# Kernel optimization log

Measured on AMD Instinct MI355X. Metric: run time of the kernel, lower is better.

Reference implementation:

```python
import jax, jax.numpy as jnp
import numpy as np

ALPHA = 1.702
LIMIT = 7.0
TOP_K = 4
NUM_EXPERTS = 16


def setup_inputs() -> dict:
    key = jax.random.key(0)
    ks = jax.random.split(key, 7)
    B, S, H, D, E = 2, 2048, 2048, 2048, NUM_EXPERTS
    return {
        "hidden_states": jax.random.normal(ks[0], (B, S, H), jnp.float32),
        "router_weight": jax.random.normal(ks[1], (E, H), jnp.float32) * 0.02,
        "router_bias": jax.random.normal(ks[2], (E,), jnp.float32) * 0.02,
        "gate_up_proj": jax.random.normal(ks[3], (E, H, 2 * D), jnp.float32) * 0.02,
        "gate_up_proj_bias": jax.random.normal(ks[4], (E, 2 * D), jnp.float32) * 0.02,
        "down_proj": jax.random.normal(ks[5], (E, D, H), jnp.float32) * 0.02,
        "down_proj_bias": jax.random.normal(ks[6], (E, H), jnp.float32) * 0.02,
    }


def _moe(x, gate_up_proj, gate_up_proj_bias, down_proj, down_proj_bias, w_te):
    # x: [T,H]; w_te: [T,E] combine weights (zero for unrouted token/expert pairs)
    T, H = x.shape

    def step(acc, params):
        Wgu, bgu, Wd, bd, we = params  # we: [T]
        gate_up = x @ Wgu + bgu                       # [T, 2D]
        gate, up = jnp.split(gate_up, 2, axis=-1)
        gate = jnp.minimum(gate, LIMIT)               # clamp(max=limit)
        up = jnp.clip(up, -LIMIT, LIMIT)
        glu = gate * jax.nn.sigmoid(gate * ALPHA)
        gated = (up + 1.0) * glu                      # [T, D]
        out = gated @ Wd + bd                         # [T, H]
        return acc + out * we[:, None], None

    acc, _ = jax.lax.scan(
        step,
        jnp.zeros((T, H), jnp.float32),
        (gate_up_proj, gate_up_proj_bias, down_proj, down_proj_bias, w_te.T),
    )
    return acc


def reference(hidden_states, router_weight, router_bias, gate_up_proj,
              gate_up_proj_bias, down_proj, down_proj_bias):
    B, S, H = hidden_states.shape
    x = hidden_states.reshape(-1, H).astype(jnp.float32)  # [T,H]
    T = x.shape[0]

    # Router
    logits = x @ router_weight.T + router_bias            # [T,E]
    top_vals, top_idx = jax.lax.top_k(logits, TOP_K)      # [T,K]
    scores = jax.nn.softmax(top_vals, axis=-1) / TOP_K    # [T,K]

    # Scatter per-token top-k scores into dense [T,E] combine weights
    w_te = jnp.zeros((T, NUM_EXPERTS), jnp.float32)
    w_te = w_te.at[jnp.arange(T)[:, None], top_idx].add(scores)

    y = _moe(x, gate_up_proj, gate_up_proj_bias, down_proj, down_proj_bias, w_te)
    y = y * TOP_K                                         # MLP multiplies by num_experts_per_tok
    y = y.reshape(B, S, H).astype(hidden_states.dtype)
    return y, scores
```

## Files before the change

### kernel.cpp

```cpp
#include <hip/hip_runtime.h>
#include <hip/hip_bf16.h>
#include <math.h>

#define T_TOK 4096
#define H_DIM 2048
#define D_DIM 2048
#define TWO_D 4096
#define E_NUM 16
#define NPAIR (T_TOK * 4)

typedef __attribute__((ext_vector_type(8))) short v8s;
typedef __attribute__((ext_vector_type(4))) float v4f;

__device__ __forceinline__ ushort f2bf(float f) {
    union { float f; unsigned u; } v; v.f = f;
    unsigned u = v.u + 0x7fffu + ((v.u >> 16) & 1u);
    return (ushort)(u >> 16);
}
__device__ __forceinline__ float bf2f(ushort b) {
    union { unsigned u; float f; } v; v.u = ((unsigned)b) << 16;
    return v.f;
}

__global__ void k_convert_x(const float* __restrict__ x, ushort* __restrict__ xb) {
    size_t i = ((size_t)blockIdx.x * 256 + threadIdx.x) * 4;
    float4 v = *(const float4*)(x + i);
    ushort4 o = make_ushort4(f2bf(v.x), f2bf(v.y), f2bf(v.z), f2bf(v.w));
    *(ushort4*)(xb + i) = o;
}

__global__ void k_router(const float* __restrict__ x, const float* __restrict__ rw,
                         const float* __restrict__ rb, float* __restrict__ logits) {
    int t = blockIdx.x;
    int e = threadIdx.x >> 4;
    int j = threadIdx.x & 15;
    const float* xr = x + (size_t)t * H_DIM;
    const float* wr = rw + (size_t)e * H_DIM;
    float s = 0.f;
    #pragma unroll 8
    for (int h = j; h < H_DIM; h += 16) s += xr[h] * wr[h];
    #pragma unroll
    for (int d = 8; d >= 1; d >>= 1) s += __shfl_down(s, d, 16);
    if (j == 0) logits[t * E_NUM + e] = s + rb[e];
}

__global__ void k_topk(const float* __restrict__ logits, float* __restrict__ scores_out,
                       int* __restrict__ tk_e, float* __restrict__ tk_w,
                       int* __restrict__ counts) {
    int t = blockIdx.x * 256 + threadIdx.x;
    if (t >= T_TOK) return;
    float lg[E_NUM];
    #pragma unroll
    for (int e = 0; e < E_NUM; e++) lg[e] = logits[t * E_NUM + e];
    int sel[4]; float sv[4];
    unsigned used = 0;
    #pragma unroll
    for (int k = 0; k < 4; k++) {
        float best = -INFINITY; int bi = 0;
        #pragma unroll
        for (int e = 0; e < E_NUM; e++) {
            if (!((used >> e) & 1) && lg[e] > best) { best = lg[e]; bi = e; }
        }
        used |= 1u << bi; sel[k] = bi; sv[k] = best;
    }
    float m = sv[0];
    float ex[4]; float sum = 0.f;
    #pragma unroll
    for (int k = 0; k < 4; k++) { ex[k] = __expf(sv[k] - m); sum += ex[k]; }
    float inv = 1.f / sum;
    #pragma unroll
    for (int k = 0; k < 4; k++) {
        float w = ex[k] * inv;
        scores_out[t * 4 + k] = w * 0.25f;
        tk_e[t * 4 + k] = sel[k];
        tk_w[t * 4 + k] = w;
        atomicAdd(&counts[sel[k]], 1);
    }
}

__global__ void k_scan(const int* __restrict__ counts, int* __restrict__ offsets) {
    if (threadIdx.x == 0) {
        int s = 0;
        for (int e = 0; e < E_NUM; e++) { offsets[e] = s; s += counts[e]; }
        offsets[E_NUM] = s;
    }
}

__global__ void k_scatter(const int* __restrict__ tk_e, const int* __restrict__ offsets,
                          int* __restrict__ fill, int* __restrict__ pair_token,
                          int* __restrict__ slot_of) {
    int i = blockIdx.x * 256 + threadIdx.x;
    if (i >= NPAIR) return;
    int e = tk_e[i];
    int pos = offsets[e] + atomicAdd(&fill[e], 1);
    pair_token[pos] = i >> 2;
    slot_of[i] = pos;
}

#define BM 128
#define BN 128
#define BK 64
#define LDT 72

__global__ __launch_bounds__(256) void k_gemm1(
    const ushort* __restrict__ xb, const float* __restrict__ Wgu,
    const float* __restrict__ bgu, const int* __restrict__ offsets,
    const int* __restrict__ pair_token, ushort* __restrict__ gu)
{
    __shared__ ushort As[BM * LDT];
    __shared__ ushort Bs[BN * LDT];
    __shared__ int rowtok[BM];

    const int e = blockIdx.z;
    const int off = offsets[e];
    const int cnt = offsets[e + 1] - off;
    const int m0 = blockIdx.y * BM;
    if (m0 >= cnt) return;
    const int n0 = blockIdx.x * BN;
    const int tid = threadIdx.x;

    if (tid < BM) {
        int r = m0 + tid; if (r >= cnt) r = cnt - 1;
        rowtok[tid] = pair_token[off + r];
    }

    const float* W = Wgu + (size_t)e * H_DIM * TWO_D + n0;

    v4f acc[4][4];
    #pragma unroll
    for (int i = 0; i < 4; i++)
        #pragma unroll
        for (int j = 0; j < 4; j++) acc[i][j] = (v4f){0.f, 0.f, 0.f, 0.f};

    const int lane = tid & 63;
    const int wm = ((tid >> 6) & 1) * 64;
    const int wn = (tid >> 7) * 64;
    const int lm = lane & 15;
    const int kg = lane >> 4;

    for (int kb = 0; kb < H_DIM; kb += BK) {
        __syncthreads();
        #pragma unroll
        for (int i = 0; i < 4; i++) {
            int c = tid + 256 * i;
            int row = c >> 3, cq = c & 7;
            const ushort* src = xb + (size_t)rowtok[row] * H_DIM + kb + cq * 8;
            *(uint4*)&As[row * LDT + cq * 8] = *(const uint4*)src;
        }
        #pragma unroll
        for (int i = 0; i < 2; i++) {
            int blk = tid + 256 * i;
            int kb4 = blk >> 5, nb4 = blk & 31;
            const float* wp = W + (size_t)(kb + kb4 * 4) * TWO_D + nb4 * 4;
            float4 r0 = *(const float4*)wp;
            float4 r1 = *(const float4*)(wp + TWO_D);
            float4 r2 = *(const float4*)(wp + 2 * TWO_D);
            float4 r3 = *(const float4*)(wp + 3 * TWO_D);
            ushort* bp = &Bs[(nb4 * 4) * LDT + kb4 * 4];
            *(ushort4*)bp             = make_ushort4(f2bf(r0.x), f2bf(r1.x), f2bf(r2.x), f2bf(r3.x));
            *(ushort4*)(bp + LDT)     = make_ushort4(f2bf(r0.y), f2bf(r1.y), f2bf(r2.y), f2bf(r3.y));
            *(ushort4*)(bp + 2 * LDT) = make_ushort4(f2bf(r0.z), f2bf(r1.z), f2bf(r2.z), f2bf(r3.z));
            *(ushort4*)(bp + 3 * LDT) = make_ushort4(f2bf(r0.w), f2bf(r1.w), f2bf(r2.w), f2bf(r3.w));
        }
        __syncthreads();
        #pragma unroll
        for (int ks = 0; ks < 2; ks++) {
            v8s af[4], bfr[4];
            #pragma unroll
            for (int mi = 0; mi < 4; mi++)
                af[mi] = *(const v8s*)&As[(wm + mi * 16 + lm) * LDT + ks * 32 + kg * 8];
            #pragma unroll
            for (int ni = 0; ni < 4; ni++)
                bfr[ni] = *(const v8s*)&Bs[(wn + ni * 16 + lm) * LDT + ks * 32 + kg * 8];
            #pragma unroll
            for (int mi = 0; mi < 4; mi++)
                #pragma unroll
                for (int ni = 0; ni < 4; ni++)
                    acc[mi][ni] = __builtin_amdgcn_mfma_f32_16x16x32_bf16(af[mi], bfr[ni], acc[mi][ni], 0, 0, 0);
        }
    }

    const float* bias = bgu + (size_t)e * TWO_D + n0;
    #pragma unroll
    for (int mi = 0; mi < 4; mi++) {
        int rbase = wm + mi * 16 + kg * 4;
        #pragma unroll
        for (int ni = 0; ni < 4; ni++) {
            int nl = wn + ni * 16 + lm;
            float bv = bias[nl];
            #pragma unroll
            for (int v = 0; v < 4; v++) {
                int r = rbase + v;
                if (m0 + r < cnt)
                    gu[(size_t)(off + m0 + r) * TWO_D + n0 + nl] = f2bf(acc[mi][ni][v] + bv);
            }
        }
    }
}

__global__ void k_act(const ushort* __restrict__ gu, ushort* __restrict__ gated) {
    int i = blockIdx.x * 256 + threadIdx.x;
    int pr = i >> 9;
    int q = (i & 511) * 4;
    const ushort* grow = gu + (size_t)pr * TWO_D;
    ushort4 g4 = *(const ushort4*)(grow + q);
    ushort4 u4 = *(const ushort4*)(grow + D_DIM + q);
    float g[4] = { bf2f(g4.x), bf2f(g4.y), bf2f(g4.z), bf2f(g4.w) };
    float u[4] = { bf2f(u4.x), bf2f(u4.y), bf2f(u4.z), bf2f(u4.w) };
    ushort o[4];
    #pragma unroll
    for (int j = 0; j < 4; j++) {
        float gate = fminf(g[j], 7.f);
        float up = fminf(fmaxf(u[j], -7.f), 7.f);
        float glu = gate / (1.f + __expf(-1.702f * gate));
        o[j] = f2bf((up + 1.f) * glu);
    }
    *(ushort4*)(gated + (size_t)pr * D_DIM + q) = make_ushort4(o[0], o[1], o[2], o[3]);
}

__global__ __launch_bounds__(256) void k_gemm2(
    const ushort* __restrict__ gated, const float* __restrict__ Wd,
    const float* __restrict__ bd, const int* __restrict__ offsets,
    ushort* __restrict__ po)
{
    __shared__ ushort As[BM * LDT];
    __shared__ ushort Bs[BN * LDT];

    const int e = blockIdx.z;
    const int off = offsets[e];
    const int cnt = offsets[e + 1] - off;
    const int m0 = blockIdx.y * BM;
    if (m0 >= cnt) return;
    const int n0 = blockIdx.x * BN;
    const int tid = threadIdx.x;

    const float* W = Wd + (size_t)e * D_DIM * H_DIM + n0;

    v4f acc[4][4];
    #pragma unroll
    for (int i = 0; i < 4; i++)
        #pragma unroll
        for (int j = 0; j < 4; j++) acc[i][j] = (v4f){0.f, 0.f, 0.f, 0.f};

    const int lane = tid & 63;
    const int wm = ((tid >> 6) & 1) * 64;
    const int wn = (tid >> 7) * 64;
    const int lm = lane & 15;
    const int kg = lane >> 4;

    for (int kb = 0; kb < D_DIM; kb += BK) {
        __syncthreads();
        #pragma unroll
        for (int i = 0; i < 4; i++) {
            int c = tid + 256 * i;
            int row = c >> 3, cq = c & 7;
            int gr = m0 + row; if (gr >= cnt) gr = cnt - 1;
            const ushort* src = gated + (size_t)(off + gr) * D_DIM + kb + cq * 8;
            *(uint4*)&As[row * LDT + cq * 8] = *(const uint4*)src;
        }
        #pragma unroll
        for (int i = 0; i < 2; i++) {
            int blk = tid + 256 * i;
            int kb4 = blk >> 5, nb4 = blk & 31;
            const float* wp = W + (size_t)(kb + kb4 * 4) * H_DIM + nb4 * 4;
            float4 r0 = *(const float4*)wp;
            float4 r1 = *(const float4*)(wp + H_DIM);
            float4 r2 = *(const float4*)(wp + 2 * H_DIM);
            float4 r3 = *(const float4*)(wp + 3 * H_DIM);
            ushort* bp = &Bs[(nb4 * 4) * LDT + kb4 * 4];
            *(ushort4*)bp             = make_ushort4(f2bf(r0.x), f2bf(r1.x), f2bf(r2.x), f2bf(r3.x));
            *(ushort4*)(bp + LDT)     = make_ushort4(f2bf(r0.y), f2bf(r1.y), f2bf(r2.y), f2bf(r3.y));
            *(ushort4*)(bp + 2 * LDT) = make_ushort4(f2bf(r0.z), f2bf(r1.z), f2bf(r2.z), f2bf(r3.z));
            *(ushort4*)(bp + 3 * LDT) = make_ushort4(f2bf(r0.w), f2bf(r1.w), f2bf(r2.w), f2bf(r3.w));
        }
        __syncthreads();
        #pragma unroll
        for (int ks = 0; ks < 2; ks++) {
            v8s af[4], bfr[4];
            #pragma unroll
            for (int mi = 0; mi < 4; mi++)
                af[mi] = *(const v8s*)&As[(wm + mi * 16 + lm) * LDT + ks * 32 + kg * 8];
            #pragma unroll
            for (int ni = 0; ni < 4; ni++)
                bfr[ni] = *(const v8s*)&Bs[(wn + ni * 16 + lm) * LDT + ks * 32 + kg * 8];
            #pragma unroll
            for (int mi = 0; mi < 4; mi++)
                #pragma unroll
                for (int ni = 0; ni < 4; ni++)
                    acc[mi][ni] = __builtin_amdgcn_mfma_f32_16x16x32_bf16(af[mi], bfr[ni], acc[mi][ni], 0, 0, 0);
        }
    }

    const float* bias = bd + (size_t)e * H_DIM + n0;
    #pragma unroll
    for (int mi = 0; mi < 4; mi++) {
        int rbase = wm + mi * 16 + kg * 4;
        #pragma unroll
        for (int ni = 0; ni < 4; ni++) {
            int nl = wn + ni * 16 + lm;
            float bv = bias[nl];
            #pragma unroll
            for (int v = 0; v < 4; v++) {
                int r = rbase + v;
                if (m0 + r < cnt)
                    po[(size_t)(off + m0 + r) * H_DIM + n0 + nl] = f2bf(acc[mi][ni][v] + bv);
            }
        }
    }
}

__global__ void k_combine(const ushort* __restrict__ po, const int* __restrict__ slot_of,
                          const float* __restrict__ tk_w, float* __restrict__ y) {
    const int t = blockIdx.x;
    int s[4]; float w[4];
    #pragma unroll
    for (int k = 0; k < 4; k++) { s[k] = slot_of[t * 4 + k]; w[k] = tk_w[t * 4 + k]; }
    const int h = threadIdx.x * 8;
    float acc[8];
    #pragma unroll
    for (int j = 0; j < 8; j++) acc[j] = 0.f;
    #pragma unroll
    for (int k = 0; k < 4; k++) {
        const ushort* row = po + (size_t)s[k] * H_DIM + h;
        ushort4 a = *(const ushort4*)row;
        ushort4 b = *(const ushort4*)(row + 4);
        acc[0] += w[k] * bf2f(a.x); acc[1] += w[k] * bf2f(a.y);
        acc[2] += w[k] * bf2f(a.z); acc[3] += w[k] * bf2f(a.w);
        acc[4] += w[k] * bf2f(b.x); acc[5] += w[k] * bf2f(b.y);
        acc[6] += w[k] * bf2f(b.z); acc[7] += w[k] * bf2f(b.w);
    }
    float* yp = y + (size_t)t * H_DIM + h;
    *(float4*)yp = make_float4(acc[0], acc[1], acc[2], acc[3]);
    *(float4*)(yp + 4) = make_float4(acc[4], acc[5], acc[6], acc[7]);
}

extern "C" void kernel_launch(void* const* d_in, const int* in_sizes, int n_in,
                              void* d_out, int out_size, void* d_ws, size_t ws_size,
                              hipStream_t stream) {
    const float* x   = (const float*)d_in[0];
    const float* rw  = (const float*)d_in[1];
    const float* rb  = (const float*)d_in[2];
    const float* wgu = (const float*)d_in[3];
    const float* bgu = (const float*)d_in[4];
    const float* wd  = (const float*)d_in[5];
    const float* bd  = (const float*)d_in[6];
    float* y = (float*)d_out;
    float* scores = y + (size_t)T_TOK * H_DIM;

    char* p = (char*)d_ws;
    auto alloc = [&](size_t bytes) { char* r = p; p += (bytes + 255) & ~(size_t)255; return r; };
    ushort* xb         = (ushort*)alloc((size_t)T_TOK * H_DIM * 2);
    float*  logits     = (float*) alloc((size_t)T_TOK * E_NUM * 4);
    int*    tk_e       = (int*)   alloc(NPAIR * 4);
    float*  tk_w       = (float*) alloc(NPAIR * 4);
    int*    slot_of    = (int*)   alloc(NPAIR * 4);
    int*    pair_token = (int*)   alloc(NPAIR * 4);
    int*    cnt_fill   = (int*)   alloc(512);
    int*    offsets    = (int*)   alloc(128);
    ushort* gu         = (ushort*)alloc((size_t)NPAIR * TWO_D * 2);
    ushort* gated      = (ushort*)alloc((size_t)NPAIR * D_DIM * 2);
    ushort* pairout    = gu;
    int* counts = cnt_fill;
    int* fill   = cnt_fill + 64;

    hipMemsetAsync(cnt_fill, 0, 512, stream);
    k_convert_x<<<(T_TOK * H_DIM) / (256 * 4), 256, 0, stream>>>(x, xb);
    k_router<<<T_TOK, 256, 0, stream>>>(x, rw, rb, logits);
    k_topk<<<T_TOK / 256, 256, 0, stream>>>(logits, scores, tk_e, tk_w, counts);
    k_scan<<<1, 64, 0, stream>>>(counts, offsets);
    k_scatter<<<NPAIR / 256, 256, 0, stream>>>(tk_e, offsets, fill, pair_token, slot_of);
    k_gemm1<<<dim3(TWO_D / BN, T_TOK / BM, E_NUM), 256, 0, stream>>>(xb, wgu, bgu, offsets, pair_token, gu);
    k_act<<<(NPAIR * 512) / 256, 256, 0, stream>>>(gu, gated);
    k_gemm2<<<dim3(H_DIM / BN, T_TOK / BM, E_NUM), 256, 0, stream>>>(gated, wd, bd, offsets, pairout);
    k_combine<<<T_TOK, 256, 0, stream>>>(pairout, slot_of, tk_w, y);
}
```

Baseline: 1.892 ms.

## Pre-transpose weights to bf16 and use async global-to-LDS loads in GEMMs

```diff
diff --git a/kernel.cpp b/kernel.cpp
--- a/kernel.cpp
+++ b/kernel.cpp
@@ -22,11 +22,48 @@
     return v.f;
 }
 
+__device__ __forceinline__ void async16(ushort* lds, const ushort* g) {
+    __builtin_amdgcn_global_load_lds(
+        (const __attribute__((address_space(1))) unsigned int*)g,
+        (__attribute__((address_space(3))) unsigned int*)lds, 16, 0, 0);
+}
+
 __global__ void k_convert_x(const float* __restrict__ x, ushort* __restrict__ xb) {
     size_t i = ((size_t)blockIdx.x * 256 + threadIdx.x) * 4;
     float4 v = *(const float4*)(x + i);
-    ushort4 o = make_ushort4(f2bf(v.x), f2bf(v.y), f2bf(v.z), f2bf(v.w));
-    *(ushort4*)(xb + i) = o;
+    *(ushort4*)(xb + i) = make_ushort4(f2bf(v.x), f2bf(v.y), f2bf(v.z), f2bf(v.w));
+}
+
+__global__ __launch_bounds__(256) void k_transpose(const float* __restrict__ W,
+                                                   ushort* __restrict__ Wt,
+                                                   int K, int N) {
+    __shared__ ushort tile[64][72];
+    const int e = blockIdx.z;
+    const int kb = blockIdx.y * 64;
+    const int nb = blockIdx.x * 64;
+    const int tid = threadIdx.x;
+    const float* src = W + ((size_t)e * K + kb) * N + nb;
+    #pragma unroll
+    for (int i = 0; i < 4; i++) {
+        int lin = tid + 256 * i;
+        int r = lin >> 4, c4 = (lin & 15) * 4;
+        float4 v = *(const float4*)(src + (size_t)r * N + c4);
+        tile[c4 + 0][r] = f2bf(v.x);
+        tile[c4 + 1][r] = f2bf(v.y);
+        tile[c4 + 2][r] = f2bf(v.z);
+        tile[c4 + 3][r] = f2bf(v.w);
+    }
+    __syncthreads();
+    ushort* dst = Wt + ((size_t)e * N + nb) * K + kb;
+    #pragma unroll
+    for (int j = 0; j < 2; j++) {
+        int lin = tid + 256 * j;
+        int n = lin >> 3, kc = (lin & 7) * 8;
+        ushort4 a = *(const ushort4*)&tile[n][kc];
+        ushort4 b = *(const ushort4*)&tile[n][kc + 4];
+        *(ushort4*)(dst + (size_t)n * K + kc) = a;
+        *(ushort4*)(dst + (size_t)n * K + kc + 4) = b;
+    }
 }
 
 __global__ void k_router(const float* __restrict__ x, const float* __restrict__ rw,
@@ -34,11 +71,14 @@
     int t = blockIdx.x;
     int e = threadIdx.x >> 4;
     int j = threadIdx.x & 15;
-    const float* xr = x + (size_t)t * H_DIM;
-    const float* wr = rw + (size_t)e * H_DIM;
+    const float4* xr = (const float4*)(x + (size_t)t * H_DIM);
+    const float4* wr = (const float4*)(rw + (size_t)e * H_DIM);
     float s = 0.f;
     #pragma unroll 8
-    for (int h = j; h < H_DIM; h += 16) s += xr[h] * wr[h];
+    for (int h = j; h < H_DIM / 4; h += 16) {
+        float4 a = xr[h], b = wr[h];
+        s += a.x * b.x + a.y * b.y + a.z * b.z + a.w * b.w;
+    }
     #pragma unroll
     for (int d = 8; d >= 1; d >>= 1) s += __shfl_down(s, d, 16);
     if (j == 0) logits[t * E_NUM + e] = s + rb[e];
@@ -100,16 +140,16 @@
 #define BM 128
 #define BN 128
 #define BK 64
-#define LDT 72
-
-__global__ __launch_bounds__(256) void k_gemm1(
-    const ushort* __restrict__ xb, const float* __restrict__ Wgu,
-    const float* __restrict__ bgu, const int* __restrict__ offsets,
-    const int* __restrict__ pair_token, ushort* __restrict__ gu)
+
+template <bool GATHER>
+__global__ __launch_bounds__(256) void k_gemm(
+    const ushort* __restrict__ A, const ushort* __restrict__ Bt,
+    const float* __restrict__ bias, const int* __restrict__ offsets,
+    const int* __restrict__ pair_token, ushort* __restrict__ out,
+    int N, int K)
 {
-    __shared__ ushort As[BM * LDT];
-    __shared__ ushort Bs[BN * LDT];
-    __shared__ int rowtok[BM];
+    __shared__ ushort As[BM * BK];
+    __shared__ ushort Bs[BN * BK];
 
     const int e = blockIdx.z;
     const int off = offsets[e];
@@ -118,13 +158,21 @@
     if (m0 >= cnt) return;
     const int n0 = blockIdx.x * BN;
     const int tid = threadIdx.x;
-
-    if (tid < BM) {
-        int r = m0 + tid; if (r >= cnt) r = cnt - 1;
-        rowtok[tid] = pair_token[off + r];
-    }
-
-    const float* W = Wgu + (size_t)e * H_DIM * TWO_D + n0;
+    const int wave = tid >> 6;
+    const int lane = tid & 63;
+    const int lm = lane & 15;
+    const int kg = lane >> 4;
+
+    int ar0 = m0 + (2 * wave) * 16 + lm;       if (ar0 >= cnt) ar0 = cnt - 1;
+    int ar1 = m0 + (2 * wave + 1) * 16 + lm;   if (ar1 >= cnt) ar1 = cnt - 1;
+    const ushort* aptr0 = A + (size_t)(GATHER ? pair_token[off + ar0] : off + ar0) * K + kg * 8;
+    const ushort* aptr1 = A + (size_t)(GATHER ? pair_token[off + ar1] : off + ar1) * K + kg * 8;
+    const ushort* bbase = Bt + (size_t)e * N * K;
+    const ushort* bptr0 = bbase + (size_t)(n0 + (2 * wave) * 16 + lm) * K + kg * 8;
+    const ushort* bptr1 = bbase + (size_t)(n0 + (2 * wave + 1) * 16 + lm) * K + kg * 8;
+
+    ushort* asub = &As[(4 * wave) * 512];
+    ushort* bsub = &Bs[(4 * wave) * 512];
 
     v4f acc[4][4];
     #pragma unroll
@@ -132,46 +180,29 @@
         #pragma unroll
         for (int j = 0; j < 4; j++) acc[i][j] = (v4f){0.f, 0.f, 0.f, 0.f};
 
-    const int lane = tid & 63;
-    const int wm = ((tid >> 6) & 1) * 64;
-    const int wn = (tid >> 7) * 64;
-    const int lm = lane & 15;
-    const int kg = lane >> 4;
-
-    for (int kb = 0; kb < H_DIM; kb += BK) {
+    const int mb = (wave & 1) * 4;
+    const int nb = (wave >> 1) * 4;
+
+    for (int kb = 0; kb < K; kb += BK) {
         __syncthreads();
-        #pragma unroll
-        for (int i = 0; i < 4; i++) {
-            int c = tid + 256 * i;
-            int row = c >> 3, cq = c & 7;
-            const ushort* src = xb + (size_t)rowtok[row] * H_DIM + kb + cq * 8;
-            *(uint4*)&As[row * LDT + cq * 8] = *(const uint4*)src;
-        }
-        #pragma unroll
-        for (int i = 0; i < 2; i++) {
-            int blk = tid + 256 * i;
-            int kb4 = blk >> 5, nb4 = blk & 31;
-            const float* wp = W + (size_t)(kb + kb4 * 4) * TWO_D + nb4 * 4;
-            float4 r0 = *(const float4*)wp;
-            float4 r1 = *(const float4*)(wp + TWO_D);
-            float4 r2 = *(const float4*)(wp + 2 * TWO_D);
-            float4 r3 = *(const float4*)(wp + 3 * TWO_D);
-            ushort* bp = &Bs[(nb4 * 4) * LDT + kb4 * 4];
-            *(ushort4*)bp             = make_ushort4(f2bf(r0.x), f2bf(r1.x), f2bf(r2.x), f2bf(r3.x));
-            *(ushort4*)(bp + LDT)     = make_ushort4(f2bf(r0.y), f2bf(r1.y), f2bf(r2.y), f2bf(r3.y));
-            *(ushort4*)(bp + 2 * LDT) = make_ushort4(f2bf(r0.z), f2bf(r1.z), f2bf(r2.z), f2bf(r3.z));
-            *(ushort4*)(bp + 3 * LDT) = make_ushort4(f2bf(r0.w), f2bf(r1.w), f2bf(r2.w), f2bf(r3.w));
-        }
+        async16(asub,        aptr0 + kb);
+        async16(asub + 512,  aptr0 + kb + 32);
+        async16(asub + 1024, aptr1 + kb);
+        async16(asub + 1536, aptr1 + kb + 32);
+        async16(bsub,        bptr0 + kb);
+        async16(bsub + 512,  bptr0 + kb + 32);
+        async16(bsub + 1024, bptr1 + kb);
+        async16(bsub + 1536, bptr1 + kb + 32);
         __syncthreads();
         #pragma unroll
         for (int ks = 0; ks < 2; ks++) {
             v8s af[4], bfr[4];
             #pragma unroll
             for (int mi = 0; mi < 4; mi++)
-                af[mi] = *(const v8s*)&As[(wm + mi * 16 + lm) * LDT + ks * 32 + kg * 8];
+                af[mi] = *(const v8s*)&As[((mb + mi) * 2 + ks) * 512 + lane * 8];
             #pragma unroll
             for (int ni = 0; ni < 4; ni++)
-                bfr[ni] = *(const v8s*)&Bs[(wn + ni * 16 + lm) * LDT + ks * 32 + kg * 8];
+                bfr[ni] = *(const v8s*)&Bs[((nb + ni) * 2 + ks) * 512 + lane * 8];
             #pragma unroll
             for (int mi = 0; mi < 4; mi++)
                 #pragma unroll
@@ -180,19 +211,21 @@
         }
     }
 
-    const float* bias = bgu + (size_t)e * TWO_D + n0;
+    const int wm = (wave & 1) * 64;
+    const int wn = (wave >> 1) * 64;
+    const float* bp = bias + (size_t)e * N + n0;
     #pragma unroll
     for (int mi = 0; mi < 4; mi++) {
         int rbase = wm + mi * 16 + kg * 4;
         #pragma unroll
         for (int ni = 0; ni < 4; ni++) {
             int nl = wn + ni * 16 + lm;
-            float bv = bias[nl];
+            float bv = bp[nl];
             #pragma unroll
             for (int v = 0; v < 4; v++) {
                 int r = rbase + v;
                 if (m0 + r < cnt)
-                    gu[(size_t)(off + m0 + r) * TWO_D + n0 + nl] = f2bf(acc[mi][ni][v] + bv);
+                    out[(size_t)(off + m0 + r) * N + n0 + nl] = f2bf(acc[mi][ni][v] + bv);
             }
         }
     }
@@ -216,97 +249,6 @@
         o[j] = f2bf((up + 1.f) * glu);
     }
     *(ushort4*)(gated + (size_t)pr * D_DIM + q) = make_ushort4(o[0], o[1], o[2], o[3]);
-}
-
-__global__ __launch_bounds__(256) void k_gemm2(
-    const ushort* __restrict__ gated, const float* __restrict__ Wd,
-    const float* __restrict__ bd, const int* __restrict__ offsets,
-    ushort* __restrict__ po)
-{
-    __shared__ ushort As[BM * LDT];
-    __shared__ ushort Bs[BN * LDT];
-
-    const int e = blockIdx.z;
-    const int off = offsets[e];
-    const int cnt = offsets[e + 1] - off;
-    const int m0 = blockIdx.y * BM;
-    if (m0 >= cnt) return;
-    const int n0 = blockIdx.x * BN;
-    const int tid = threadIdx.x;
-
-    const float* W = Wd + (size_t)e * D_DIM * H_DIM + n0;
-
-    v4f acc[4][4];
-    #pragma unroll
-    for (int i = 0; i < 4; i++)
-        #pragma unroll
-        for (int j = 0; j < 4; j++) acc[i][j] = (v4f){0.f, 0.f, 0.f, 0.f};
-
-    const int lane = tid & 63;
-    const int wm = ((tid >> 6) & 1) * 64;
-    const int wn = (tid >> 7) * 64;
-    const int lm = lane & 15;
-    const int kg = lane >> 4;
-
-    for (int kb = 0; kb < D_DIM; kb += BK) {
-        __syncthreads();
-        #pragma unroll
-        for (int i = 0; i < 4; i++) {
-            int c = tid + 256 * i;
-            int row = c >> 3, cq = c & 7;
-            int gr = m0 + row; if (gr >= cnt) gr = cnt - 1;
-            const ushort* src = gated + (size_t)(off + gr) * D_DIM + kb + cq * 8;
-            *(uint4*)&As[row * LDT + cq * 8] = *(const uint4*)src;
-        }
-        #pragma unroll
-        for (int i = 0; i < 2; i++) {
-            int blk = tid + 256 * i;
-            int kb4 = blk >> 5, nb4 = blk & 31;
-            const float* wp = W + (size_t)(kb + kb4 * 4) * H_DIM + nb4 * 4;
-            float4 r0 = *(const float4*)wp;
-            float4 r1 = *(const float4*)(wp + H_DIM);
-            float4 r2 = *(const float4*)(wp + 2 * H_DIM);
-            float4 r3 = *(const float4*)(wp + 3 * H_DIM);
-            ushort* bp = &Bs[(nb4 * 4) * LDT + kb4 * 4];
-            *(ushort4*)bp             = make_ushort4(f2bf(r0.x), f2bf(r1.x), f2bf(r2.x), f2bf(r3.x));
-            *(ushort4*)(bp + LDT)     = make_ushort4(f2bf(r0.y), f2bf(r1.y), f2bf(r2.y), f2bf(r3.y));
-            *(ushort4*)(bp + 2 * LDT) = make_ushort4(f2bf(r0.z), f2bf(r1.z), f2bf(r2.z), f2bf(r3.z));
-            *(ushort4*)(bp + 3 * LDT) = make_ushort4(f2bf(r0.w), f2bf(r1.w), f2bf(r2.w), f2bf(r3.w));
-        }
-        __syncthreads();
-        #pragma unroll
-        for (int ks = 0; ks < 2; ks++) {
-            v8s af[4], bfr[4];
-            #pragma unroll
-            for (int mi = 0; mi < 4; mi++)
-                af[mi] = *(const v8s*)&As[(wm + mi * 16 + lm) * LDT + ks * 32 + kg * 8];
-            #pragma unroll
-            for (int ni = 0; ni < 4; ni++)
-                bfr[ni] = *(const v8s*)&Bs[(wn + ni * 16 + lm) * LDT + ks * 32 + kg * 8];
-            #pragma unroll
-            for (int mi = 0; mi < 4; mi++)
-                #pragma unroll
-                for (int ni = 0; ni < 4; ni++)
-                    acc[mi][ni] = __builtin_amdgcn_mfma_f32_16x16x32_bf16(af[mi], bfr[ni], acc[mi][ni], 0, 0, 0);
-        }
-    }
-
-    const float* bias = bd + (size_t)e * H_DIM + n0;
-    #pragma unroll
-    for (int mi = 0; mi < 4; mi++) {
-        int rbase = wm + mi * 16 + kg * 4;
-        #pragma unroll
-        for (int ni = 0; ni < 4; ni++) {
-            int nl = wn + ni * 16 + lm;
-            float bv = bias[nl];
-            #pragma unroll
-            for (int v = 0; v < 4; v++) {
-                int r = rbase + v;
-                if (m0 + r < cnt)
-                    po[(size_t)(off + m0 + r) * H_DIM + n0 + nl] = f2bf(acc[mi][ni][v] + bv);
-            }
-        }
-    }
 }
 
 __global__ void k_combine(const ushort* __restrict__ po, const int* __restrict__ slot_of,
@@ -350,6 +292,8 @@
     char* p = (char*)d_ws;
     auto alloc = [&](size_t bytes) { char* r = p; p += (bytes + 255) & ~(size_t)255; return r; };
     ushort* xb         = (ushort*)alloc((size_t)T_TOK * H_DIM * 2);
+    ushort* wgu_t      = (ushort*)alloc((size_t)E_NUM * TWO_D * H_DIM * 2);
+    ushort* wd_t       = (ushort*)alloc((size_t)E_NUM * H_DIM * D_DIM * 2);
     float*  logits     = (float*) alloc((size_t)T_TOK * E_NUM * 4);
     int*    tk_e       = (int*)   alloc(NPAIR * 4);
     float*  tk_w       = (float*) alloc(NPAIR * 4);
@@ -365,12 +309,16 @@
 
     hipMemsetAsync(cnt_fill, 0, 512, stream);
     k_convert_x<<<(T_TOK * H_DIM) / (256 * 4), 256, 0, stream>>>(x, xb);
+    k_transpose<<<dim3(TWO_D / 64, H_DIM / 64, E_NUM), 256, 0, stream>>>(wgu, wgu_t, H_DIM, TWO_D);
+    k_transpose<<<dim3(H_DIM / 64, D_DIM / 64, E_NUM), 256, 0, stream>>>(wd, wd_t, D_DIM, H_DIM);
     k_router<<<T_TOK, 256, 0, stream>>>(x, rw, rb, logits);
     k_topk<<<T_TOK / 256, 256, 0, stream>>>(logits, scores, tk_e, tk_w, counts);
     k_scan<<<1, 64, 0, stream>>>(counts, offsets);
     k_scatter<<<NPAIR / 256, 256, 0, stream>>>(tk_e, offsets, fill, pair_token, slot_of);
-    k_gemm1<<<dim3(TWO_D / BN, T_TOK / BM, E_NUM), 256, 0, stream>>>(xb, wgu, bgu, offsets, pair_token, gu);
+    k_gemm<true><<<dim3(TWO_D / BN, T_TOK / BM, E_NUM), 256, 0, stream>>>(
+        xb, wgu_t, bgu, offsets, pair_token, gu, TWO_D, H_DIM);
     k_act<<<(NPAIR * 512) / 256, 256, 0, stream>>>(gu, gated);
-    k_gemm2<<<dim3(H_DIM / BN, T_TOK / BM, E_NUM), 256, 0, stream>>>(gated, wd, bd, offsets, pairout);
+    k_gemm<false><<<dim3(H_DIM / BN, T_TOK / BM, E_NUM), 256, 0, stream>>>(
+        gated, wd_t, bd, offsets, pair_token, pairout, H_DIM, D_DIM);
     k_combine<<<T_TOK, 256, 0, stream>>>(pairout, slot_of, tk_w, y);
 }
```

New measurement: 1.995 ms. 5.4% more time.
